# Kernel tuning notes

Measured on AMD Instinct MI355X. Metric: run time of the kernel, lower is better.

## Reference

```python
import jax, jax.numpy as jnp
import numpy as np


def setup_inputs() -> dict:
    key = jax.random.key(0)
    kq, kk, kv = jax.random.split(key, 3)
    B, L, S, H, E = 2, 2048, 2048, 16, 64
    queries = jax.random.normal(kq, (B, L, H, E), dtype=jnp.float32)
    keys = jax.random.normal(kk, (B, S, H, E), dtype=jnp.float32)
    values = jax.random.normal(kv, (B, S, H, E), dtype=jnp.float32)
    # TriangularCausalMask: True strictly above the diagonal (positions to mask)
    causal = jnp.triu(jnp.ones((L, S), dtype=jnp.bool_), k=1)
    attn_mask = jnp.broadcast_to(causal[None, None, :, :], (B, 1, L, S))
    return {"queries": queries, "keys": keys, "values": values, "attn_mask": attn_mask}


def reference(queries, keys, values, attn_mask):
    # queries: [B,L,H,E], keys/values: [B,S,H,E], attn_mask: [B,1,L,S] bool
    E = queries.shape[-1]
    scale = 1.0 / jnp.sqrt(jnp.asarray(E, dtype=queries.dtype))
    scores = jnp.einsum('blhe,bshe->bhls', queries, keys)      # [B,H,L,S]
    scores = jnp.where(attn_mask, -jnp.inf, scores)
    A = jax.nn.softmax(scale * scores, axis=-1)                # dropout is identity in eval
    V = jnp.einsum('bhls,bshd->blhd', A, values)               # [B,L,H,D]
    return V, A
```

## Files before the change

kernel.cpp:

```cpp
#include <hip/hip_runtime.h>
#include <hip/hip_bf16.h>


#define B_ 2
#define L_ 2048
#define S_ 2048
#define H_ 16
#define E_ 64
#define HE 1024
#define KP 72
#define PP 68
#define NT 32

typedef __attribute__((ext_vector_type(8))) __bf16 bfrag;
typedef __attribute__((ext_vector_type(4))) float f32x4;

__device__ __forceinline__ unsigned short f2bu(float x) {
    __bf16 b = (__bf16)x;
    return __builtin_bit_cast(unsigned short, b);
}

__device__ __forceinline__ void barrier_nodrain() {
    asm volatile("s_waitcnt lgkmcnt(0)" ::: "memory");
    __builtin_amdgcn_s_barrier();
    __builtin_amdgcn_sched_barrier(0);
}

__global__ __launch_bounds__(512, 4)
void fullattn_kernel(const float* __restrict__ Qg,
                     const float* __restrict__ Kg,
                     const float* __restrict__ Vg,
                     float* __restrict__ Vout,
                     float* __restrict__ Aout)
{
    __shared__ __align__(16) __bf16 Ks[64 * KP];
    __shared__ __align__(16) __bf16 Vt[64 * KP];
    __shared__ __align__(16) float  Pw[8][16 * PP];

    const int tid  = threadIdx.x;
    const int wave = tid >> 6;
    const int half = wave >> 2;
    const int wv   = wave & 3;
    const int lane = tid & 63;
    const int ln   = lane & 15;
    const int quad = lane >> 4;
    const int lq   = quad * 4;

    const int p   = blockIdx.x;
    const int qt  = half ? (NT - 1 - p) : p;
    const int qtB = NT - 1 - p;
    const int bh  = blockIdx.y;
    const int b   = bh >> 4;
    const int h   = bh & 15;

    const int q0w = qt * 64 + wv * 16;

    const float* qbase = Qg + ((size_t)b * L_ * H_ + h) * E_;
    const float* kbase = Kg + ((size_t)b * S_ * H_ + h) * E_;
    const float* vbase = Vg + ((size_t)b * S_ * H_ + h) * E_;
    float* arow0 = Aout + (size_t)bh * L_ * S_;

    bfrag qf[2];
    {
        const float* qr = qbase + (size_t)(q0w + ln) * HE;
        #pragma unroll
        for (int kc = 0; kc < 2; ++kc) {
            const float* pq = qr + kc * 32 + quad * 8;
            float4 a0 = *(const float4*)(pq);
            float4 a1 = *(const float4*)(pq + 4);
            bfrag f;
            f[0] = (__bf16)(a0.x * 0.125f); f[1] = (__bf16)(a0.y * 0.125f);
            f[2] = (__bf16)(a0.z * 0.125f); f[3] = (__bf16)(a0.w * 0.125f);
            f[4] = (__bf16)(a1.x * 0.125f); f[5] = (__bf16)(a1.y * 0.125f);
            f[6] = (__bf16)(a1.z * 0.125f); f[7] = (__bf16)(a1.w * 0.125f);
            qf[kc] = f;
        }
    }

    const int r  = tid >> 3;
    const int c0 = tid & 7;

    float lsum[4] = {0.f, 0.f, 0.f, 0.f};

    float4 kpre[2];
    {
        const float* kr = kbase + (size_t)r * HE;
        #pragma unroll
        for (int i = 0; i < 2; ++i)
            kpre[i] = *(const float4*)(kr + (c0 + i * 8) * 4);
    }

    for (int st = 0; st <= qtB; ++st) {
        #pragma unroll
        for (int i = 0; i < 2; ++i) {
            int f4 = c0 + i * 8;
            ushort4 kb;
            kb.x = f2bu(kpre[i].x); kb.y = f2bu(kpre[i].y);
            kb.z = f2bu(kpre[i].z); kb.w = f2bu(kpre[i].w);
            *(ushort4*)&Ks[r * KP + f4 * 4] = kb;
        }
        if (st < qtB) {
            const float* kr = kbase + (size_t)((st + 1) * 64 + r) * HE;
            #pragma unroll
            for (int i = 0; i < 2; ++i)
                kpre[i] = *(const float4*)(kr + (c0 + i * 8) * 4);
        }
        barrier_nodrain();

        if (st <= qt) {
            #pragma unroll
            for (int nc = 0; nc < 4; ++nc) {
                f32x4 acc = {0.f, 0.f, 0.f, 0.f};
                __builtin_amdgcn_s_setprio(1);
                #pragma unroll
                for (int kc = 0; kc < 2; ++kc) {
                    bfrag bk = *(const bfrag*)&Ks[(nc * 16 + ln) * KP + kc * 32 + quad * 8];
                    acc = __builtin_amdgcn_mfma_f32_16x16x32_bf16(qf[kc], bk, acc, 0, 0, 0);
                }
                __builtin_amdgcn_s_setprio(0);
                const int s_abs = st * 64 + nc * 16 + ln;
                #pragma unroll
                for (int rg = 0; rg < 4; ++rg) {
                    const int q_abs = q0w + lq + rg;
                    float e = (s_abs <= q_abs) ? __expf(acc[rg]) : 0.0f;
                    lsum[rg] += e;
                }
            }
        }
        barrier_nodrain();
    }

    float4 kp2[2], vp2[2];
    {
        const float* kr = kbase + (size_t)r * HE;
        const float* vr = vbase + (size_t)r * HE;
        #pragma unroll
        for (int i = 0; i < 2; ++i) {
            kp2[i] = *(const float4*)(kr + (c0 + i * 8) * 4);
            vp2[i] = *(const float4*)(vr + (c0 + i * 8) * 4);
        }
    }

    float inv_l[4];
    #pragma unroll
    for (int rg = 0; rg < 4; ++rg) {
        float v = lsum[rg];
        v += __shfl_xor(v, 1);
        v += __shfl_xor(v, 2);
        v += __shfl_xor(v, 4);
        v += __shfl_xor(v, 8);
        inv_l[rg] = 1.0f / v;
    }

    f32x4 oacc[4];
    #pragma unroll
    for (int dc = 0; dc < 4; ++dc) {
        f32x4 z = {0.f, 0.f, 0.f, 0.f};
        oacc[dc] = z;
    }

    const int wr = lane >> 2;
    const int wc = (lane & 3) * 4;
    int zf = qt + 1;

    for (int st = 0; st <= qtB; ++st) {
        #pragma unroll
        for (int i = 0; i < 2; ++i) {
            int f4 = c0 + i * 8;
            ushort4 kb;
            kb.x = f2bu(kp2[i].x); kb.y = f2bu(kp2[i].y);
            kb.z = f2bu(kp2[i].z); kb.w = f2bu(kp2[i].w);
            *(ushort4*)&Ks[r * KP + f4 * 4] = kb;
            const int d0 = f4 * 4;
            Vt[(d0 + 0) * KP + r] = (__bf16)vp2[i].x;
            Vt[(d0 + 1) * KP + r] = (__bf16)vp2[i].y;
            Vt[(d0 + 2) * KP + r] = (__bf16)vp2[i].z;
            Vt[(d0 + 3) * KP + r] = (__bf16)vp2[i].w;
        }
        if (st < qtB) {
            const float* kr = kbase + (size_t)((st + 1) * 64 + r) * HE;
            const float* vr = vbase + (size_t)((st + 1) * 64 + r) * HE;
            #pragma unroll
            for (int i = 0; i < 2; ++i) {
                kp2[i] = *(const float4*)(kr + (c0 + i * 8) * 4);
                vp2[i] = *(const float4*)(vr + (c0 + i * 8) * 4);
            }
        }
        barrier_nodrain();

        if (st <= qt) {
            #pragma unroll
            for (int nc = 0; nc < 4; ++nc) {
                f32x4 acc = {0.f, 0.f, 0.f, 0.f};
                __builtin_amdgcn_s_setprio(1);
                #pragma unroll
                for (int kc = 0; kc < 2; ++kc) {
                    bfrag bk = *(const bfrag*)&Ks[(nc * 16 + ln) * KP + kc * 32 + quad * 8];
                    acc = __builtin_amdgcn_mfma_f32_16x16x32_bf16(qf[kc], bk, acc, 0, 0, 0);
                }
                __builtin_amdgcn_s_setprio(0);
                const int s_abs = st * 64 + nc * 16 + ln;
                #pragma unroll
                for (int rg = 0; rg < 4; ++rg) {
                    const int q_abs = q0w + lq + rg;
                    float e = (s_abs <= q_abs) ? __expf(acc[rg]) : 0.0f;
                    Pw[wave][(lq + rg) * PP + nc * 16 + ln] = e * inv_l[rg];
                }
            }
            bfrag af[2];
            #pragma unroll
            for (int kc = 0; kc < 2; ++kc) {
                const float* pp = &Pw[wave][ln * PP + kc * 32 + quad * 8];
                float4 p0 = *(const float4*)pp;
                float4 p1 = *(const float4*)(pp + 4);
                bfrag f;
                f[0] = (__bf16)p0.x; f[1] = (__bf16)p0.y;
                f[2] = (__bf16)p0.z; f[3] = (__bf16)p0.w;
                f[4] = (__bf16)p1.x; f[5] = (__bf16)p1.y;
                f[6] = (__bf16)p1.z; f[7] = (__bf16)p1.w;
                af[kc] = f;
            }

            #pragma unroll
            for (int dc = 0; dc < 4; ++dc) {
                __builtin_amdgcn_s_setprio(1);
                #pragma unroll
                for (int kc = 0; kc < 2; ++kc) {
                    bfrag bv = *(const bfrag*)&Vt[(dc * 16 + ln) * KP + kc * 32 + quad * 8];
                    oacc[dc] = __builtin_amdgcn_mfma_f32_16x16x32_bf16(af[kc], bv, oacc[dc], 0, 0, 0);
                }
                __builtin_amdgcn_s_setprio(0);
            }

            float* ar = arow0 + (size_t)(q0w + wr) * S_ + st * 64;
            #pragma unroll
            for (int c4 = 0; c4 < 4; ++c4) {
                float4 v4 = *(const float4*)&Pw[wave][wr * PP + wc + c4 * 16];
                *(float4*)(ar + wc + c4 * 16) = v4;
            }
        } else if (zf < NT) {
            const float4 z4 = {0.f, 0.f, 0.f, 0.f};
            float* ar = arow0 + (size_t)(q0w + wr) * S_ + zf * 64;
            #pragma unroll
            for (int c4 = 0; c4 < 4; ++c4)
                *(float4*)(ar + wc + c4 * 16) = z4;
            ++zf;
        }
        barrier_nodrain();
    }

    {
        const float4 z4 = {0.f, 0.f, 0.f, 0.f};
        for (; zf < NT; ++zf) {
            float* ar = arow0 + (size_t)(q0w + wr) * S_ + zf * 64;
            #pragma unroll
            for (int c4 = 0; c4 < 4; ++c4)
                *(float4*)(ar + wc + c4 * 16) = z4;
        }
    }

    #pragma unroll
    for (int rg = 0; rg < 4; ++rg) {
        float* vr = Vout + ((size_t)(b * L_ + q0w + lq + rg) * H_ + h) * E_;
        #pragma unroll
        for (int dc = 0; dc < 4; ++dc)
            vr[dc * 16 + ln] = oacc[dc][rg];
    }
}

extern "C" void kernel_launch(void* const* d_in, const int* in_sizes, int n_in,
                              void* d_out, int out_size, void* d_ws, size_t ws_size,
                              hipStream_t stream) {
    const float* Q = (const float*)d_in[0];
    const float* K = (const float*)d_in[1];
    const float* V = (const float*)d_in[2];
    float* out  = (float*)d_out;
    float* Vo   = out;
    float* Ao   = out + (size_t)B_ * L_ * H_ * E_;
    dim3 grid(NT / 2, B_ * H_);
    fullattn_kernel<<<grid, 512, 0, stream>>>(Q, K, V, Vo, Ao);
}
```

Baseline: 667.3 us.

## Double-buffer K/V LDS tiles and move zero-fill of masked A into pass one

K and V tiles in shared memory are now double-buffered, so the next tile is written into the alternate buffer while the current one is consumed. This removes one barrier per iteration in both the row-sum pass and the output pass. Writing zeros to the fully masked attention blocks moves into the first pass, where idle waves would otherwise wait. Block-to-tile mapping is also rotated by head group to spread load, at the cost of doubling LDS for K/V, which may reduce occupancy.

```diff
diff --git a/kernel.cpp b/kernel.cpp
--- a/kernel.cpp
+++ b/kernel.cpp
@@ -33,8 +33,8 @@
                      float* __restrict__ Vout,
                      float* __restrict__ Aout)
 {
-    __shared__ __align__(16) __bf16 Ks[64 * KP];
-    __shared__ __align__(16) __bf16 Vt[64 * KP];
+    __shared__ __align__(16) __bf16 Ks[2][64 * KP];
+    __shared__ __align__(16) __bf16 Vt[2][64 * KP];
     __shared__ __align__(16) float  Pw[8][16 * PP];
 
     const int tid  = threadIdx.x;
@@ -46,13 +46,14 @@
     const int quad = lane >> 4;
     const int lq   = quad * 4;
 
-    const int p   = blockIdx.x;
+    const int bx = blockIdx.x;
+    const int bh = blockIdx.y;
+    const int p  = (bx + ((bh & 16) ? 8 : 0)) & 15;
+    const int b  = bh >> 4;
+    const int h  = bh & 15;
+
     const int qt  = half ? (NT - 1 - p) : p;
     const int qtB = NT - 1 - p;
-    const int bh  = blockIdx.y;
-    const int b   = bh >> 4;
-    const int h   = bh & 15;
-
     const int q0w = qt * 64 + wv * 16;
 
     const float* qbase = Qg + ((size_t)b * L_ * H_ + h) * E_;
@@ -80,8 +81,12 @@
     const int r  = tid >> 3;
     const int c0 = tid & 7;
 
+    const int wr = lane >> 2;
+    const int wc = (lane & 3) * 4;
+
+    int zf = qt + 1;
+
     float lsum[4] = {0.f, 0.f, 0.f, 0.f};
-
     float4 kpre[2];
     {
         const float* kr = kbase + (size_t)r * HE;
@@ -89,24 +94,40 @@
         for (int i = 0; i < 2; ++i)
             kpre[i] = *(const float4*)(kr + (c0 + i * 8) * 4);
     }
+    #pragma unroll
+    for (int i = 0; i < 2; ++i) {
+        int f4 = c0 + i * 8;
+        ushort4 kb;
+        kb.x = f2bu(kpre[i].x); kb.y = f2bu(kpre[i].y);
+        kb.z = f2bu(kpre[i].z); kb.w = f2bu(kpre[i].w);
+        *(ushort4*)&Ks[0][r * KP + f4 * 4] = kb;
+    }
+    if (qtB >= 1) {
+        const float* kr = kbase + (size_t)(64 + r) * HE;
+        #pragma unroll
+        for (int i = 0; i < 2; ++i)
+            kpre[i] = *(const float4*)(kr + (c0 + i * 8) * 4);
+    }
+    barrier_nodrain();
 
     for (int st = 0; st <= qtB; ++st) {
-        #pragma unroll
-        for (int i = 0; i < 2; ++i) {
-            int f4 = c0 + i * 8;
-            ushort4 kb;
-            kb.x = f2bu(kpre[i].x); kb.y = f2bu(kpre[i].y);
-            kb.z = f2bu(kpre[i].z); kb.w = f2bu(kpre[i].w);
-            *(ushort4*)&Ks[r * KP + f4 * 4] = kb;
-        }
+        const int cb = st & 1;
         if (st < qtB) {
-            const float* kr = kbase + (size_t)((st + 1) * 64 + r) * HE;
-            #pragma unroll
-            for (int i = 0; i < 2; ++i)
-                kpre[i] = *(const float4*)(kr + (c0 + i * 8) * 4);
-        }
-        barrier_nodrain();
-
+            #pragma unroll
+            for (int i = 0; i < 2; ++i) {
+                int f4 = c0 + i * 8;
+                ushort4 kb;
+                kb.x = f2bu(kpre[i].x); kb.y = f2bu(kpre[i].y);
+                kb.z = f2bu(kpre[i].z); kb.w = f2bu(kpre[i].w);
+                *(ushort4*)&Ks[cb ^ 1][r * KP + f4 * 4] = kb;
+            }
+            if (st + 1 < qtB) {
+                const float* kr = kbase + (size_t)((st + 2) * 64 + r) * HE;
+                #pragma unroll
+                for (int i = 0; i < 2; ++i)
+                    kpre[i] = *(const float4*)(kr + (c0 + i * 8) * 4);
+            }
+        }
         if (st <= qt) {
             #pragma unroll
             for (int nc = 0; nc < 4; ++nc) {
@@ -114,7 +135,7 @@
                 __builtin_amdgcn_s_setprio(1);
                 #pragma unroll
                 for (int kc = 0; kc < 2; ++kc) {
-                    bfrag bk = *(const bfrag*)&Ks[(nc * 16 + ln) * KP + kc * 32 + quad * 8];
+                    bfrag bk = *(const bfrag*)&Ks[cb][(nc * 16 + ln) * KP + kc * 32 + quad * 8];
                     acc = __builtin_amdgcn_mfma_f32_16x16x32_bf16(qf[kc], bk, acc, 0, 0, 0);
                 }
                 __builtin_amdgcn_s_setprio(0);
@@ -126,6 +147,13 @@
                     lsum[rg] += e;
                 }
             }
+        } else if (zf < NT) {
+            const float4 z4 = {0.f, 0.f, 0.f, 0.f};
+            float* ar = arow0 + (size_t)(q0w + wr) * S_ + zf * 64;
+            #pragma unroll
+            for (int c4 = 0; c4 < 4; ++c4)
+                *(float4*)(ar + wc + c4 * 16) = z4;
+            ++zf;
         }
         barrier_nodrain();
     }
@@ -159,34 +187,56 @@
         oacc[dc] = z;
     }
 
-    const int wr = lane >> 2;
-    const int wc = (lane & 3) * 4;
-    int zf = qt + 1;
+    #pragma unroll
+    for (int i = 0; i < 2; ++i) {
+        int f4 = c0 + i * 8;
+        ushort4 kb;
+        kb.x = f2bu(kp2[i].x); kb.y = f2bu(kp2[i].y);
+        kb.z = f2bu(kp2[i].z); kb.w = f2bu(kp2[i].w);
+        *(ushort4*)&Ks[0][r * KP + f4 * 4] = kb;
+        const int d0 = f4 * 4;
+        Vt[0][(d0 + 0) * KP + r] = (__bf16)vp2[i].x;
+        Vt[0][(d0 + 1) * KP + r] = (__bf16)vp2[i].y;
+        Vt[0][(d0 + 2) * KP + r] = (__bf16)vp2[i].z;
+        Vt[0][(d0 + 3) * KP + r] = (__bf16)vp2[i].w;
+    }
+    if (qtB >= 1) {
+        const float* kr = kbase + (size_t)(64 + r) * HE;
+        const float* vr = vbase + (size_t)(64 + r) * HE;
+        #pragma unroll
+        for (int i = 0; i < 2; ++i) {
+            kp2[i] = *(const float4*)(kr + (c0 + i * 8) * 4);
+            vp2[i] = *(const float4*)(vr + (c0 + i * 8) * 4);
+        }
+    }
+    barrier_nodrain();
 
     for (int st = 0; st <= qtB; ++st) {
-        #pragma unroll
-        for (int i = 0; i < 2; ++i) {
-            int f4 = c0 + i * 8;
-            ushort4 kb;
-            kb.x = f2bu(kp2[i].x); kb.y = f2bu(kp2[i].y);
-            kb.z = f2bu(kp2[i].z); kb.w = f2bu(kp2[i].w);
-            *(ushort4*)&Ks[r * KP + f4 * 4] = kb;
-            const int d0 = f4 * 4;
-            Vt[(d0 + 0) * KP + r] = (__bf16)vp2[i].x;
-            Vt[(d0 + 1) * KP + r] = (__bf16)vp2[i].y;
-            Vt[(d0 + 2) * KP + r] = (__bf16)vp2[i].z;
-            Vt[(d0 + 3) * KP + r] = (__bf16)vp2[i].w;
-        }
+        const int cb = st & 1;
         if (st < qtB) {
-            const float* kr = kbase + (size_t)((st + 1) * 64 + r) * HE;
-            const float* vr = vbase + (size_t)((st + 1) * 64 + r) * HE;
             #pragma unroll
             for (int i = 0; i < 2; ++i) {
-                kp2[i] = *(const float4*)(kr + (c0 + i * 8) * 4);
-                vp2[i] = *(const float4*)(vr + (c0 + i * 8) * 4);
-            }
-        }
-        barrier_nodrain();
+                int f4 = c0 + i * 8;
+                ushort4 kb;
+                kb.x = f2bu(kp2[i].x); kb.y = f2bu(kp2[i].y);
+                kb.z = f2bu(kp2[i].z); kb.w = f2bu(kp2[i].w);
+                *(ushort4*)&Ks[cb ^ 1][r * KP + f4 * 4] = kb;
+                const int d0 = f4 * 4;
+                Vt[cb ^ 1][(d0 + 0) * KP + r] = (__bf16)vp2[i].x;
+                Vt[cb ^ 1][(d0 + 1) * KP + r] = (__bf16)vp2[i].y;
+                Vt[cb ^ 1][(d0 + 2) * KP + r] = (__bf16)vp2[i].z;
+                Vt[cb ^ 1][(d0 + 3) * KP + r] = (__bf16)vp2[i].w;
+            }
+            if (st + 1 < qtB) {
+                const float* kr = kbase + (size_t)((st + 2) * 64 + r) * HE;
+                const float* vr = vbase + (size_t)((st + 2) * 64 + r) * HE;
+                #pragma unroll
+                for (int i = 0; i < 2; ++i) {
+                    kp2[i] = *(const float4*)(kr + (c0 + i * 8) * 4);
+                    vp2[i] = *(const float4*)(vr + (c0 + i * 8) * 4);
+                }
+            }
+        }
 
         if (st <= qt) {
             #pragma unroll
@@ -195,7 +245,7 @@
                 __builtin_amdgcn_s_setprio(1);
                 #pragma unroll
                 for (int kc = 0; kc < 2; ++kc) {
-                    bfrag bk = *(const bfrag*)&Ks[(nc * 16 + ln) * KP + kc * 32 + quad * 8];
+                    bfrag bk = *(const bfrag*)&Ks[cb][(nc * 16 + ln) * KP + kc * 32 + quad * 8];
                     acc = __builtin_amdgcn_mfma_f32_16x16x32_bf16(qf[kc], bk, acc, 0, 0, 0);
                 }
                 __builtin_amdgcn_s_setprio(0);
@@ -220,18 +270,16 @@
                 f[6] = (__bf16)p1.z; f[7] = (__bf16)p1.w;
                 af[kc] = f;
             }
-
             #pragma unroll
             for (int dc = 0; dc < 4; ++dc) {
                 __builtin_amdgcn_s_setprio(1);
                 #pragma unroll
                 for (int kc = 0; kc < 2; ++kc) {
-                    bfrag bv = *(const bfrag*)&Vt[(dc * 16 + ln) * KP + kc * 32 + quad * 8];
+                    bfrag bv = *(const bfrag*)&Vt[cb][(dc * 16 + ln) * KP + kc * 32 + quad * 8];
                     oacc[dc] = __builtin_amdgcn_mfma_f32_16x16x32_bf16(af[kc], bv, oacc[dc], 0, 0, 0);
                 }
                 __builtin_amdgcn_s_setprio(0);
             }
-
             float* ar = arow0 + (size_t)(q0w + wr) * S_ + st * 64;
             #pragma unroll
             for (int c4 = 0; c4 < 4; ++c4) {
@@ -274,9 +322,9 @@
     const float* Q = (const float*)d_in[0];
     const float* K = (const float*)d_in[1];
     const float* V = (const float*)d_in[2];
-    float* out  = (float*)d_out;
-    float* Vo   = out;
-    float* Ao   = out + (size_t)B_ * L_ * H_ * E_;
-    dim3 grid(NT / 2, B_ * H_);
+    float* out = (float*)d_out;
+    float* Vo  = out;
+    float* Ao  = out + (size_t)B_ * L_ * H_ * E_;
+    dim3 grid(16, B_ * H_);
     fullattn_kernel<<<grid, 512, 0, stream>>>(Q, K, V, Vo, Ao);
 }
```

Measured after the change: 680.4 us. Within noise of the previous version (+2.0%).
